# Performance work log

Measured on AMD Instinct MI355X. Metric: run time of the kernel, lower is better.

The kernel has to match this reference:

```python
import jax, jax.numpy as jnp
import numpy as np

B, N, C, CS, CP, H, L = 1, 2048, 128, 128, 16, 4, 3
NQ, NK = 32, 128  # local attention window: n_queries, n_keys
EPS = 1e-5


def _make_beta(n):
    l = np.arange(n)[:, None]
    m = np.arange(n)[None, :]
    con = np.zeros((n, n), dtype=bool)
    for c in np.arange(NQ / 2, n, NQ):
        con |= (np.abs(l - c) < NQ / 2) & (np.abs(m - c) < NK / 2)
    return np.where(con, 0.0, -1e10).astype(np.float32)


def setup_inputs() -> dict:
    key = jax.random.key(0)
    ks = iter(jax.random.split(key, 32))
    w = lambda *shape: jax.random.normal(next(ks), shape, dtype=jnp.float32) * 0.02
    inp = {
        'a': jax.random.normal(next(ks), (B, N, C), dtype=jnp.float32),
        's': jax.random.normal(next(ks), (B, N, CS), dtype=jnp.float32),
        'z': jax.random.normal(next(ks), (B, N, N, CP), dtype=jnp.float32),
        'beta': jnp.asarray(_make_beta(N))[None],
        'ada1_ln_w': jnp.ones((L, CS)), 'ada1_lin_w': w(L, CS, C),
        'ada1_lin_b': jnp.zeros((L, C)), 'ada1_nb_w': w(L, CS, C),
        'lnz_w': jnp.ones((L, CP)), 'lnz_b': jnp.zeros((L, CP)),
        'zinj_w': w(L, CP, H),
        'q_w': w(L, C, C), 'q_b': jnp.zeros((L, C)),
        'k_w': w(L, C, C), 'v_w': w(L, C, C),
        'g_w': w(L, C, C), 'o_w': w(L, C, C),
        'agate_w': w(L, CS, C), 'agate_b': jnp.full((L, C), -2.0),
        'ada2_ln_w': jnp.ones((L, CS)), 'ada2_lin_w': w(L, CS, C),
        'ada2_lin_b': jnp.zeros((L, C)), 'ada2_nb_w': w(L, CS, C),
        'lin1_w': w(L, C, 2 * C), 'lin2_w': w(L, C, 2 * C), 'lin3_w': w(L, 2 * C, C),
        'tgate_w': w(L, CS, C), 'tgate_b': jnp.full((L, C), -2.0),
    }
    return inp


def _ln(x):
    mu = jnp.mean(x, axis=-1, keepdims=True)
    var = jnp.var(x, axis=-1, keepdims=True)
    return (x - mu) * jax.lax.rsqrt(var + EPS)


def _adaln(a, s, ln_w, lin_w, lin_b, nb_w):
    # AdaLN: LN(a) gated & shifted by LN(s)
    a = _ln(a)
    sn = _ln(s) * ln_w
    return jax.nn.sigmoid(sn @ lin_w + lin_b) * a + sn @ nb_w


def _forward(a, s, z, beta, ada1_ln_w, ada1_lin_w, ada1_lin_b, ada1_nb_w,
             lnz_w, lnz_b, zinj_w, q_w, q_b, k_w, v_w, g_w, o_w,
             agate_w, agate_b, ada2_ln_w, ada2_lin_w, ada2_lin_b, ada2_nb_w,
             lin1_w, lin2_w, lin3_w, tgate_w, tgate_b):
    b_, n_, c_ = a.shape
    h_ = zinj_w.shape[-1]
    d_ = c_ // h_
    scale = 1.0 / np.sqrt(d_).astype(np.float32)
    zn0 = _ln(z)  # shared pre-affine LN of pair rep
    for i in range(q_w.shape[0]):
        # --- AttentionPairBias ---
        ah = _adaln(a, s, ada1_ln_w[i], ada1_lin_w[i], ada1_lin_b[i], ada1_nb_w[i])
        zb = jnp.einsum('bijc,ch->bhij', zn0 * lnz_w[i] + lnz_b[i], zinj_w[i])
        q = ((ah @ q_w[i] + q_b[i]) * scale).reshape(b_, n_, h_, d_)
        k = (ah @ k_w[i]).reshape(b_, n_, h_, d_)
        v = (ah @ v_w[i]).reshape(b_, n_, h_, d_)
        scores = jnp.einsum('bihd,bjhd->bhij', q, k) + zb + beta[:, None]
        p = jax.nn.softmax(scores, axis=-1)
        o = jnp.einsum('bhij,bjhd->bihd', p, v).reshape(b_, n_, c_)
        o = o * jax.nn.sigmoid(ah @ g_w[i])
        attn = (o @ o_w[i]) * jax.nn.sigmoid(s @ agate_w[i] + agate_b[i])
        # --- ConditionedTransitionBlock ---
        th = _adaln(a, s, ada2_ln_w[i], ada2_lin_w[i], ada2_lin_b[i], ada2_nb_w[i])
        bb = jax.nn.silu(th @ lin1_w[i]) * (th @ lin2_w[i])
        trans = jax.nn.sigmoid(s @ tgate_w[i] + tgate_b[i]) * th * (bb @ lin3_w[i])
        a = attn + trans
    return a


def reference(a, s, z, beta, ada1_ln_w, ada1_lin_w, ada1_lin_b, ada1_nb_w,
              lnz_w, lnz_b, zinj_w, q_w, q_b, k_w, v_w, g_w, o_w,
              agate_w, agate_b, ada2_ln_w, ada2_lin_w, ada2_lin_b, ada2_nb_w,
              lin1_w, lin2_w, lin3_w, tgate_w, tgate_b):
    return _forward(a, s, z, beta, ada1_ln_w, ada1_lin_w, ada1_lin_b, ada1_nb_w,
                    lnz_w, lnz_b, zinj_w, q_w, q_b, k_w, v_w, g_w, o_w,
                    agate_w, agate_b, ada2_ln_w, ada2_lin_w, ada2_lin_b, ada2_nb_w,
                    lin1_w, lin2_w, lin3_w, tgate_w, tgate_b)
```

## Files before the change

### kernel.cpp

```cpp
#include <hip/hip_runtime.h>


#define NT 2048

__device__ __forceinline__ float sig_(float x) { return 1.0f / (1.0f + __expf(-x)); }

__device__ __forceinline__ float redsum32(float v) {
#pragma unroll
  for (int o = 16; o > 0; o >>= 1) v += __shfl_xor(v, o);
  return v;
}

__device__ __forceinline__ void mm4(const float* __restrict__ W, int ldw,
                                    const float* As_row, int K, int c0, float* acc) {
  const float* __restrict__ wp = W + c0;
  for (int k = 0; k < K; k += 4) {
    float4 a4 = *(const float4*)(As_row + k);
#pragma unroll
    for (int kk = 0; kk < 4; ++kk) {
      float a = ((const float*)&a4)[kk];
      float4 w0 = *(const float4*)(wp);
      acc[0] = fmaf(a, w0.x, acc[0]);
      acc[1] = fmaf(a, w0.y, acc[1]);
      acc[2] = fmaf(a, w0.z, acc[2]);
      acc[3] = fmaf(a, w0.w, acc[3]);
      wp += ldw;
    }
  }
}

__device__ __forceinline__ void mm4x2(const float* __restrict__ W1,
                                      const float* __restrict__ W2, int ldw,
                                      const float* As_row, int K, int c0,
                                      float* acc1, float* acc2) {
  const float* __restrict__ wp1 = W1 + c0;
  const float* __restrict__ wp2 = W2 + c0;
  for (int k = 0; k < K; k += 4) {
    float4 a4 = *(const float4*)(As_row + k);
#pragma unroll
    for (int kk = 0; kk < 4; ++kk) {
      float a = ((const float*)&a4)[kk];
      float4 w0 = *(const float4*)(wp1);
      float4 u0 = *(const float4*)(wp2);
      acc1[0] = fmaf(a, w0.x, acc1[0]);
      acc1[1] = fmaf(a, w0.y, acc1[1]);
      acc1[2] = fmaf(a, w0.z, acc1[2]);
      acc1[3] = fmaf(a, w0.w, acc1[3]);
      acc2[0] = fmaf(a, u0.x, acc2[0]);
      acc2[1] = fmaf(a, u0.y, acc2[1]);
      acc2[2] = fmaf(a, u0.z, acc2[2]);
      acc2[3] = fmaf(a, u0.w, acc2[3]);
      wp1 += ldw; wp2 += ldw;
    }
  }
}

__device__ __forceinline__ void mm2(const float* __restrict__ W, int ldw,
                                    const float* As_row, int K, int c0, float* acc) {
  const float* __restrict__ wp = W + c0;
  for (int k = 0; k < K; k += 4) {
    float4 a4 = *(const float4*)(As_row + k);
#pragma unroll
    for (int kk = 0; kk < 4; ++kk) {
      float a = ((const float*)&a4)[kk];
      float2 w0 = *(const float2*)(wp);
      acc[0] = fmaf(a, w0.x, acc[0]);
      acc[1] = fmaf(a, w0.y, acc[1]);
      wp += ldw;
    }
  }
}

__global__ __launch_bounds__(256) void k_gates(
    const float* __restrict__ s, const float* __restrict__ agw,
    const float* __restrict__ agb, const float* __restrict__ tgw,
    const float* __restrict__ tgb, float* __restrict__ gatesA,
    float* __restrict__ gatesT) {
  __shared__ float As[8 * 132];
  int r0 = blockIdx.x * 8;
  int bz = blockIdx.y;
  int l = bz % 3, which = bz / 3;
  const float* W = (which ? tgw : agw) + (size_t)l * 128 * 128;
  const float* bias = (which ? tgb : agb) + (size_t)l * 128;
  float* outp = (which ? gatesT : gatesA) + (size_t)l * NT * 128;
  int tid = threadIdx.x;
  int r = tid >> 5, sub = tid & 31;
  *(float4*)&As[r * 132 + sub * 4] =
      *(const float4*)(s + (size_t)(r0 + r) * 128 + sub * 4);
  __syncthreads();
  int c0 = sub << 2;
  float acc[4] = {0, 0, 0, 0};
  mm4(W, 128, &As[r * 132], 128, c0, acc);
  size_t base = (size_t)(r0 + r) * 128 + c0;
#pragma unroll
  for (int j = 0; j < 4; ++j) outp[base + j] = sig_(acc[j] + bias[c0 + j]);
}

__global__ __launch_bounds__(256) void k_adaln12(
    const float* __restrict__ a, const float* __restrict__ s_in,
    const float* __restrict__ lnw1, const float* __restrict__ linw1,
    const float* __restrict__ linb1, const float* __restrict__ nbw1,
    const float* __restrict__ lnw2, const float* __restrict__ linw2,
    const float* __restrict__ linb2, const float* __restrict__ nbw2,
    float* __restrict__ ah, float* __restrict__ th) {
  __shared__ float Sn[8 * 132];
  __shared__ float La[8 * 132];
  int r0 = blockIdx.x * 8;
  int y = blockIdx.y;
  const float* lnw  = y ? lnw2 : lnw1;
  const float* linw = y ? linw2 : linw1;
  const float* linb = y ? linb2 : linb1;
  const float* nbw  = y ? nbw2 : nbw1;
  float* outp = y ? th : ah;
  int tid = threadIdx.x;
  int r = tid >> 5, sub = tid & 31;
  {
    float4 x = *(const float4*)(s_in + (size_t)(r0 + r) * 128 + sub * 4);
    float sm = redsum32(x.x + x.y + x.z + x.w);
    float mu = sm * (1.0f / 128.0f);
    float4 d = make_float4(x.x - mu, x.y - mu, x.z - mu, x.w - mu);
    float v = redsum32(d.x * d.x + d.y * d.y + d.z * d.z + d.w * d.w);
    float rs = rsqrtf(v * (1.0f / 128.0f) + 1e-5f);
    float4 sc = *(const float4*)(lnw + sub * 4);
    d.x *= rs * sc.x; d.y *= rs * sc.y; d.z *= rs * sc.z; d.w *= rs * sc.w;
    *(float4*)&Sn[r * 132 + sub * 4] = d;
  }
  {
    float4 x = *(const float4*)(a + (size_t)(r0 + r) * 128 + sub * 4);
    float sm = redsum32(x.x + x.y + x.z + x.w);
    float mu = sm * (1.0f / 128.0f);
    float4 d = make_float4(x.x - mu, x.y - mu, x.z - mu, x.w - mu);
    float v = redsum32(d.x * d.x + d.y * d.y + d.z * d.z + d.w * d.w);
    float rs = rsqrtf(v * (1.0f / 128.0f) + 1e-5f);
    d.x *= rs; d.y *= rs; d.z *= rs; d.w *= rs;
    *(float4*)&La[r * 132 + sub * 4] = d;
  }
  __syncthreads();
  int c0 = sub << 2;
  float acc1[4] = {0, 0, 0, 0}, acc2[4] = {0, 0, 0, 0};
  mm4x2(linw, nbw, 128, &Sn[r * 132], 128, c0, acc1, acc2);
  size_t base = (size_t)(r0 + r) * 128 + c0;
#pragma unroll
  for (int j = 0; j < 4; ++j) {
    float g = sig_(acc1[j] + linb[c0 + j]);
    outp[base + j] = g * La[r * 132 + c0 + j] + acc2[j];
  }
}

__global__ __launch_bounds__(256) void k_proj6(
    const float* __restrict__ ah, const float* __restrict__ th,
    const float* __restrict__ qw, const float* __restrict__ kw,
    const float* __restrict__ vw, const float* __restrict__ gw,
    const float* __restrict__ qb, const float* __restrict__ w1,
    const float* __restrict__ w2, float* __restrict__ qkvg,
    float* __restrict__ bb) {
  __shared__ float As[8 * 132];
  int r0 = blockIdx.x * 8;
  int y = blockIdx.y;
  int tid = threadIdx.x;
  int r = tid >> 5, sub = tid & 31;
  const float* src = (y < 4) ? ah : th;
  *(float4*)&As[r * 132 + sub * 4] =
      *(const float4*)(src + (size_t)(r0 + r) * 128 + sub * 4);
  __syncthreads();
  if (y < 4) {
    const float* W = (y == 0) ? qw : (y == 1) ? kw : (y == 2) ? vw : gw;
    int c0 = sub << 2;
    float acc[4] = {0, 0, 0, 0};
    mm4(W, 128, &As[r * 132], 128, c0, acc);
    float* op = qkvg + (size_t)(r0 + r) * 512 + y * 128 + c0;
    if (y == 0) {
#pragma unroll
      for (int j = 0; j < 4; ++j)
        op[j] = (acc[j] + qb[c0 + j]) * 0.17677669529663687f;
    } else if (y == 3) {
#pragma unroll
      for (int j = 0; j < 4; ++j) op[j] = sig_(acc[j]);
    } else {
#pragma unroll
      for (int j = 0; j < 4; ++j) op[j] = acc[j];
    }
  } else {
    int cb0 = (y - 4) * 128;
    int c0 = cb0 + (sub << 2);
    float acc1[4] = {0, 0, 0, 0}, acc2[4] = {0, 0, 0, 0};
    mm4x2(w1, w2, 256, &As[r * 132], 128, c0, acc1, acc2);
    size_t base = (size_t)(r0 + r) * 256 + c0;
#pragma unroll
    for (int j = 0; j < 4; ++j) {
      float x1 = acc1[j];
      bb[base + j] = x1 * sig_(x1) * acc2[j];
    }
  }
}

__global__ __launch_bounds__(256) void k_wattn(
    const float* __restrict__ qkvg, const float* __restrict__ z,
    const float* __restrict__ lnzw, const float* __restrict__ lnzb,
    const float* __restrict__ zinj, float* __restrict__ og,
    float* __restrict__ colpart) {
  __shared__ float Qs[8][128];
  __shared__ float S[8][4][132];
  __shared__ float KV[32][128];
  __shared__ float wz[4][16];
  __shared__ float bzw[2][4];
  __shared__ float red[2][128];

  const int tid = threadIdx.x;
  const int bx = blockIdx.x;
  if (bx >= 256) {
    int b = bx - 256;
    int rr = tid >> 7, c = tid & 127;
    float acc = 0.0f;
    for (int t = 0; t < 16; ++t) {
      int row = b * 32 + rr + t * 2;
      acc += qkvg[(size_t)row * 512 + 256 + c];
    }
    red[rr][c] = acc;
    __syncthreads();
    if (rr == 0) colpart[b * 128 + c] = red[0][c] + red[1][c];
    return;
  }

  const int win = bx >> 2, sub4 = bx & 3;
  const int cen = 16 + 32 * win;
  const int i0 = cen - 15 + 8 * sub4;
  const int nrows = (sub4 == 3) ? 7 : 8;
  const int jlo = max(0, cen - 63), jhi = min(2047, cen + 63);
  const int nk = jhi - jlo + 1;

  if (tid < 64) {
    int h = tid & 3, c = tid >> 2;
    wz[h][c] = lnzw[c] * zinj[c * 4 + h];
  }
  if (tid < 8) {
    int h = tid & 3, which = tid >> 2;
    float acc = 0.0f;
    for (int c = 0; c < 16; ++c) acc += (which ? lnzb[c] : lnzw[c]) * zinj[c * 4 + h];
    bzw[which][h] = acc;
  }
  {
    int r = tid >> 5, sub = tid & 31;
    int i = i0 + min(r, nrows - 1);
    *(float4*)&Qs[r][sub * 4] = *(const float4*)(qkvg + (size_t)i * 512 + sub * 4);
  }
  __syncthreads();

  for (int idx = tid; idx < 8 * 128; idx += 256) {
    int r = idx >> 7, jj = idx & 127;
    if (jj < nk) {
      int i = i0 + min(r, nrows - 1);
      int j = jlo + jj;
      const float* zp = z + ((size_t)i * 2048 + j) * 16;
      float x[16];
      *(float4*)&x[0]  = *(const float4*)(zp + 0);
      *(float4*)&x[4]  = *(const float4*)(zp + 4);
      *(float4*)&x[8]  = *(const float4*)(zp + 8);
      *(float4*)&x[12] = *(const float4*)(zp + 12);
      float sm = 0.0f;
#pragma unroll
      for (int c = 0; c < 16; ++c) sm += x[c];
      float mu = sm * (1.0f / 16.0f);
      float var = 0.0f;
#pragma unroll
      for (int c = 0; c < 16; ++c) { float d = x[c] - mu; var = fmaf(d, d, var); }
      float rs = rsqrtf(var * (1.0f / 16.0f) + 1e-5f);
#pragma unroll
      for (int h = 0; h < 4; ++h) {
        float dot = 0.0f;
#pragma unroll
        for (int c = 0; c < 16; ++c) dot = fmaf(x[c], wz[h][c], dot);
        S[r][h][jj] = fmaf(rs, dot - mu * bzw[0][h], bzw[1][h]);
      }
    } else {
#pragma unroll
      for (int h = 0; h < 4; ++h) S[r][h][jj] = -1e30f;
    }
  }
  __syncthreads();

  {
    const int r = tid >> 5, h = (tid >> 3) & 3, part = tid & 7;
    float qreg[32];
#pragma unroll
    for (int d4 = 0; d4 < 32; d4 += 4)
      *(float4*)&qreg[d4] = *(const float4*)&Qs[r][h * 32 + d4];
    for (int kb = 0; kb < 128; kb += 32) {
      for (int idx = tid; idx < 32 * 32; idx += 256) {
        int kk = idx >> 5, c4 = (idx & 31) << 2;
        int j = jlo + kb + kk;
        int cs = (c4 + ((kk >> 3) << 2)) & 127;
        float4 val = make_float4(0.f, 0.f, 0.f, 0.f);
        if (j <= jhi) val = *(const float4*)(qkvg + (size_t)j * 512 + 128 + c4);
        *(float4*)&KV[kk][cs] = val;
      }
      __syncthreads();
#pragma unroll
      for (int u = 0; u < 4; ++u) {
        int jj = part + (u << 3);
        int rot = (jj >> 3) << 2;
        float dot = 0.0f;
#pragma unroll
        for (int d4 = 0; d4 < 32; d4 += 4) {
          int cs = (h * 32 + d4 + rot) & 127;
          float4 kv = *(const float4*)&KV[jj][cs];
          dot = fmaf(qreg[d4 + 0], kv.x, dot);
          dot = fmaf(qreg[d4 + 1], kv.y, dot);
          dot = fmaf(qreg[d4 + 2], kv.z, dot);
          dot = fmaf(qreg[d4 + 3], kv.w, dot);
        }
        S[r][h][kb + jj] += dot;
      }
      __syncthreads();
    }
  }

  {
    const int rh = tid >> 3, part = tid & 7;
    const int sr = rh >> 2, sh = rh & 3;
    float* Srow = &S[sr][sh][0];
    float m = -1e30f;
#pragma unroll
    for (int st = 0; st < 16; ++st) m = fmaxf(m, Srow[part + (st << 3)]);
#pragma unroll
    for (int o = 4; o > 0; o >>= 1) m = fmaxf(m, __shfl_xor(m, o));
    float ss = 0.0f;
#pragma unroll
    for (int st = 0; st < 16; ++st) {
      int jj = part + (st << 3);
      float e = __expf(Srow[jj] - m);
      Srow[jj] = e;
      ss += e;
    }
#pragma unroll
    for (int o = 4; o > 0; o >>= 1) ss += __shfl_xor(ss, o);
    float inv = 1.0f / ss;
#pragma unroll
    for (int st = 0; st < 16; ++st) Srow[part + (st << 3)] *= inv;
  }
  __syncthreads();

  {
    const int r = tid >> 5, cg = tid & 31;
    const int ca = cg << 2;
    const int h = cg >> 3;
    float acc[4] = {0, 0, 0, 0};
    for (int kb = 0; kb < 128; kb += 32) {
      for (int idx = tid; idx < 32 * 32; idx += 256) {
        int kk = idx >> 5, c4 = (idx & 31) << 2;
        int j = jlo + kb + kk;
        int cs = (c4 + ((kk >> 3) << 2)) & 127;
        float4 val = make_float4(0.f, 0.f, 0.f, 0.f);
        if (j <= jhi) val = *(const float4*)(qkvg + (size_t)j * 512 + 256 + c4);
        *(float4*)&KV[kk][cs] = val;
      }
      __syncthreads();
#pragma unroll 4
      for (int kk = 0; kk < 32; ++kk) {
        int rot = (kk >> 3) << 2;
        float sa = S[r][h][kb + kk];
        float4 va = *(const float4*)&KV[kk][(ca + rot) & 127];
        acc[0] = fmaf(sa, va.x, acc[0]);
        acc[1] = fmaf(sa, va.y, acc[1]);
        acc[2] = fmaf(sa, va.z, acc[2]);
        acc[3] = fmaf(sa, va.w, acc[3]);
      }
      __syncthreads();
    }
    if (r < nrows) {
      int i = i0 + r;
      float4 ga = *(const float4*)(qkvg + (size_t)i * 512 + 384 + ca);
      float4 oa = make_float4(acc[0] * ga.x, acc[1] * ga.y, acc[2] * ga.z, acc[3] * ga.w);
      *(float4*)(og + (size_t)i * 128 + ca) = oa;
    }
  }
}

__global__ __launch_bounds__(512) void k_tail(
    const float* __restrict__ og, const float* __restrict__ ow,
    const float* __restrict__ gA, const float* __restrict__ colpart,
    const float* __restrict__ qkvg, const float* __restrict__ bbuf,
    const float* __restrict__ w3, const float* __restrict__ gT,
    const float* __restrict__ th, float* __restrict__ outp) {
  __shared__ float Ao[8 * 132];
  __shared__ float Bb[8 * 260];
  __shared__ float red[2][128];
  int r0 = blockIdx.x * 8;
  int tid = threadIdx.x;
  int r = tid >> 6, sub = tid & 63;
  if (sub < 32) {
    *(float4*)&Ao[r * 132 + sub * 4] =
        *(const float4*)(og + (size_t)(r0 + r) * 128 + sub * 4);
  }
  {
    *(float4*)&Bb[r * 260 + sub * 4] =
        *(const float4*)(bbuf + (size_t)(r0 + r) * 256 + sub * 4);
  }
  __syncthreads();
  if ((r0 & 31) == 0) {
    if (tid < 256) {
      int col = tid & 127, half = tid >> 7;
      float acc = 0.0f;
      for (int b = half; b < 64; b += 2) acc += colpart[b * 128 + col];
      red[half][col] = acc;
    }
    __syncthreads();
    if (tid < 128) {
      float mv = (red[0][tid] + red[1][tid]) * (1.0f / 2048.0f);
      Ao[tid] = mv * qkvg[(size_t)r0 * 512 + 384 + tid];
    }
    __syncthreads();
  }
  int c0 = sub << 1;
  float acc1[2] = {0, 0};
  mm2(ow, 128, &Ao[r * 132], 128, c0, acc1);
  float acc3[2] = {0, 0};
  mm2(w3, 128, &Bb[r * 260], 256, c0, acc3);
  size_t base = (size_t)(r0 + r) * 128 + c0;
#pragma unroll
  for (int j = 0; j < 2; ++j) {
    float attnv = acc1[j] * gA[base + j];
    outp[base + j] = attnv + gT[base + j] * th[base + j] * acc3[j];
  }
}

extern "C" void kernel_launch(void* const* d_in, const int* in_sizes, int n_in,
                              void* d_out, int out_size, void* d_ws, size_t ws_size,
                              hipStream_t stream) {
  (void)in_sizes; (void)n_in; (void)out_size; (void)ws_size;
  const float* A_in   = (const float*)d_in[0];
  const float* S_in   = (const float*)d_in[1];
  const float* Z_in   = (const float*)d_in[2];
  const float* ada1_ln_w  = (const float*)d_in[4];
  const float* ada1_lin_w = (const float*)d_in[5];
  const float* ada1_lin_b = (const float*)d_in[6];
  const float* ada1_nb_w  = (const float*)d_in[7];
  const float* lnz_w      = (const float*)d_in[8];
  const float* lnz_b      = (const float*)d_in[9];
  const float* zinj_w     = (const float*)d_in[10];
  const float* q_w        = (const float*)d_in[11];
  const float* q_b        = (const float*)d_in[12];
  const float* k_w        = (const float*)d_in[13];
  const float* v_w        = (const float*)d_in[14];
  const float* g_w        = (const float*)d_in[15];
  const float* o_w        = (const float*)d_in[16];
  const float* agate_w    = (const float*)d_in[17];
  const float* agate_b    = (const float*)d_in[18];
  const float* ada2_ln_w  = (const float*)d_in[19];
  const float* ada2_lin_w = (const float*)d_in[20];
  const float* ada2_lin_b = (const float*)d_in[21];
  const float* ada2_nb_w  = (const float*)d_in[22];
  const float* lin1_w     = (const float*)d_in[23];
  const float* lin2_w     = (const float*)d_in[24];
  const float* lin3_w     = (const float*)d_in[25];
  const float* tgate_w    = (const float*)d_in[26];
  const float* tgate_b    = (const float*)d_in[27];

  const int N = NT, C = 128;
  float* ws = (float*)d_ws;
  float* ah      = ws;
  float* th      = ah + (size_t)N * C;
  float* qkvg    = th + (size_t)N * C;
  float* og      = qkvg + (size_t)N * 512;
  float* bb      = og + (size_t)N * C;
  float* gatesA  = bb + (size_t)N * 256;
  float* gatesT  = gatesA + (size_t)3 * N * C;
  float* colpart = gatesT + (size_t)3 * N * C;

  dim3 blk(256);
  k_gates<<<dim3(256, 6), blk, 0, stream>>>(S_in, agate_w, agate_b, tgate_w,
                                            tgate_b, gatesA, gatesT);
  const float* acur = A_in;
  for (int l = 0; l < 3; ++l) {
    k_adaln12<<<dim3(256, 2), blk, 0, stream>>>(
        acur, S_in, ada1_ln_w + (size_t)l * C, ada1_lin_w + (size_t)l * C * C,
        ada1_lin_b + (size_t)l * C, ada1_nb_w + (size_t)l * C * C,
        ada2_ln_w + (size_t)l * C, ada2_lin_w + (size_t)l * C * C,
        ada2_lin_b + (size_t)l * C, ada2_nb_w + (size_t)l * C * C, ah, th);
    k_proj6<<<dim3(256, 6), blk, 0, stream>>>(
        ah, th, q_w + (size_t)l * C * C, k_w + (size_t)l * C * C,
        v_w + (size_t)l * C * C, g_w + (size_t)l * C * C, q_b + (size_t)l * C,
        lin1_w + (size_t)l * C * 2 * C, lin2_w + (size_t)l * C * 2 * C, qkvg, bb);
    k_wattn<<<320, blk, 0, stream>>>(qkvg, Z_in, lnz_w + (size_t)l * 16,
                                     lnz_b + (size_t)l * 16,
                                     zinj_w + (size_t)l * 64, og, colpart);
    k_tail<<<256, dim3(512), 0, stream>>>(og, o_w + (size_t)l * C * C,
                                          gatesA + (size_t)l * N * C, colpart,
                                          qkvg, bb, lin3_w + (size_t)l * 2 * C * C,
                                          gatesT + (size_t)l * N * C, th,
                                          (float*)d_out);
    acur = (const float*)d_out;
  }
}
```

Before: 730.5 us.

## Fuse AdaLN into projection kernel and halve attention rows per block

Merges the AdaLN kernel into the QKVG/transition projection kernel. Each of the six y-blocks recomputes its needed AdaLN output (ah or th) in shared memory instead of round-tripping it through global memory, which removes one launch per layer. This adds redundant AdaLN matmuls, since four blocks recompute ah and two recompute th. Separately, the windowed attention kernel now uses 4 query rows per block over 512 blocks, with 64-key tiles, to raise parallelism at the cost of more redundant z/K/V loads per row.

```diff
diff --git a/kernel.cpp b/kernel.cpp
--- a/kernel.cpp
+++ b/kernel.cpp
@@ -96,24 +96,29 @@
   for (int j = 0; j < 4; ++j) outp[base + j] = sig_(acc[j] + bias[c0 + j]);
 }
 
-__global__ __launch_bounds__(256) void k_adaln12(
+__global__ __launch_bounds__(256) void k_projf(
     const float* __restrict__ a, const float* __restrict__ s_in,
-    const float* __restrict__ lnw1, const float* __restrict__ linw1,
-    const float* __restrict__ linb1, const float* __restrict__ nbw1,
-    const float* __restrict__ lnw2, const float* __restrict__ linw2,
-    const float* __restrict__ linb2, const float* __restrict__ nbw2,
-    float* __restrict__ ah, float* __restrict__ th) {
+    const float* __restrict__ a1lnw, const float* __restrict__ a1linw,
+    const float* __restrict__ a1linb, const float* __restrict__ a1nbw,
+    const float* __restrict__ a2lnw, const float* __restrict__ a2linw,
+    const float* __restrict__ a2linb, const float* __restrict__ a2nbw,
+    const float* __restrict__ qw, const float* __restrict__ kw,
+    const float* __restrict__ vw, const float* __restrict__ gw,
+    const float* __restrict__ qb, const float* __restrict__ w1,
+    const float* __restrict__ w2, float* __restrict__ qkvg,
+    float* __restrict__ bb, float* __restrict__ th_out) {
   __shared__ float Sn[8 * 132];
   __shared__ float La[8 * 132];
+  __shared__ float Ah[8 * 132];
   int r0 = blockIdx.x * 8;
   int y = blockIdx.y;
-  const float* lnw  = y ? lnw2 : lnw1;
-  const float* linw = y ? linw2 : linw1;
-  const float* linb = y ? linb2 : linb1;
-  const float* nbw  = y ? nbw2 : nbw1;
-  float* outp = y ? th : ah;
   int tid = threadIdx.x;
   int r = tid >> 5, sub = tid & 31;
+  const bool is2 = (y >= 4);
+  const float* lnw  = is2 ? a2lnw : a1lnw;
+  const float* linw = is2 ? a2linw : a1linw;
+  const float* linb = is2 ? a2linb : a1linb;
+  const float* nbw  = is2 ? a2nbw : a1nbw;
   {
     float4 x = *(const float4*)(s_in + (size_t)(r0 + r) * 128 + sub * 4);
     float sm = redsum32(x.x + x.y + x.z + x.w);
@@ -137,37 +142,27 @@
   }
   __syncthreads();
   int c0 = sub << 2;
-  float acc1[4] = {0, 0, 0, 0}, acc2[4] = {0, 0, 0, 0};
-  mm4x2(linw, nbw, 128, &Sn[r * 132], 128, c0, acc1, acc2);
-  size_t base = (size_t)(r0 + r) * 128 + c0;
-#pragma unroll
-  for (int j = 0; j < 4; ++j) {
-    float g = sig_(acc1[j] + linb[c0 + j]);
-    outp[base + j] = g * La[r * 132 + c0 + j] + acc2[j];
-  }
-}
-
-__global__ __launch_bounds__(256) void k_proj6(
-    const float* __restrict__ ah, const float* __restrict__ th,
-    const float* __restrict__ qw, const float* __restrict__ kw,
-    const float* __restrict__ vw, const float* __restrict__ gw,
-    const float* __restrict__ qb, const float* __restrict__ w1,
-    const float* __restrict__ w2, float* __restrict__ qkvg,
-    float* __restrict__ bb) {
-  __shared__ float As[8 * 132];
-  int r0 = blockIdx.x * 8;
-  int y = blockIdx.y;
-  int tid = threadIdx.x;
-  int r = tid >> 5, sub = tid & 31;
-  const float* src = (y < 4) ? ah : th;
-  *(float4*)&As[r * 132 + sub * 4] =
-      *(const float4*)(src + (size_t)(r0 + r) * 128 + sub * 4);
+  {
+    float acc1[4] = {0, 0, 0, 0}, acc2[4] = {0, 0, 0, 0};
+    mm4x2(linw, nbw, 128, &Sn[r * 132], 128, c0, acc1, acc2);
+    float hv[4];
+#pragma unroll
+    for (int j = 0; j < 4; ++j) {
+      float g = sig_(acc1[j] + linb[c0 + j]);
+      hv[j] = g * La[r * 132 + c0 + j] + acc2[j];
+    }
+    *(float4*)&Ah[r * 132 + c0] = make_float4(hv[0], hv[1], hv[2], hv[3]);
+    if (y == 4) {
+      size_t base = (size_t)(r0 + r) * 128 + c0;
+#pragma unroll
+      for (int j = 0; j < 4; ++j) th_out[base + j] = hv[j];
+    }
+  }
   __syncthreads();
   if (y < 4) {
     const float* W = (y == 0) ? qw : (y == 1) ? kw : (y == 2) ? vw : gw;
-    int c0 = sub << 2;
     float acc[4] = {0, 0, 0, 0};
-    mm4(W, 128, &As[r * 132], 128, c0, acc);
+    mm4(W, 128, &Ah[r * 132], 128, c0, acc);
     float* op = qkvg + (size_t)(r0 + r) * 512 + y * 128 + c0;
     if (y == 0) {
 #pragma unroll
@@ -182,10 +177,10 @@
     }
   } else {
     int cb0 = (y - 4) * 128;
-    int c0 = cb0 + (sub << 2);
+    int cc0 = cb0 + c0;
     float acc1[4] = {0, 0, 0, 0}, acc2[4] = {0, 0, 0, 0};
-    mm4x2(w1, w2, 256, &As[r * 132], 128, c0, acc1, acc2);
-    size_t base = (size_t)(r0 + r) * 256 + c0;
+    mm4x2(w1, w2, 256, &Ah[r * 132], 128, cc0, acc1, acc2);
+    size_t base = (size_t)(r0 + r) * 256 + cc0;
 #pragma unroll
     for (int j = 0; j < 4; ++j) {
       float x1 = acc1[j];
@@ -199,17 +194,17 @@
     const float* __restrict__ lnzw, const float* __restrict__ lnzb,
     const float* __restrict__ zinj, float* __restrict__ og,
     float* __restrict__ colpart) {
-  __shared__ float Qs[8][128];
-  __shared__ float S[8][4][132];
-  __shared__ float KV[32][128];
+  __shared__ float Qs[4][128];
+  __shared__ float S[4][4][132];
+  __shared__ float KV[64][128];
   __shared__ float wz[4][16];
   __shared__ float bzw[2][4];
   __shared__ float red[2][128];
 
   const int tid = threadIdx.x;
   const int bx = blockIdx.x;
-  if (bx >= 256) {
-    int b = bx - 256;
+  if (bx >= 512) {
+    int b = bx - 512;
     int rr = tid >> 7, c = tid & 127;
     float acc = 0.0f;
     for (int t = 0; t < 16; ++t) {
@@ -222,10 +217,10 @@
     return;
   }
 
-  const int win = bx >> 2, sub4 = bx & 3;
+  const int win = bx >> 3, sub8 = bx & 7;
   const int cen = 16 + 32 * win;
-  const int i0 = cen - 15 + 8 * sub4;
-  const int nrows = (sub4 == 3) ? 7 : 8;
+  const int i0 = cen - 15 + 4 * sub8;
+  const int nrows = (sub8 == 7) ? 3 : 4;
   const int jlo = max(0, cen - 63), jhi = min(2047, cen + 63);
   const int nk = jhi - jlo + 1;
 
@@ -239,14 +234,14 @@
     for (int c = 0; c < 16; ++c) acc += (which ? lnzb[c] : lnzw[c]) * zinj[c * 4 + h];
     bzw[which][h] = acc;
   }
-  {
+  if (tid < 128) {
     int r = tid >> 5, sub = tid & 31;
     int i = i0 + min(r, nrows - 1);
     *(float4*)&Qs[r][sub * 4] = *(const float4*)(qkvg + (size_t)i * 512 + sub * 4);
   }
   __syncthreads();
 
-  for (int idx = tid; idx < 8 * 128; idx += 256) {
+  for (int idx = tid; idx < 4 * 128; idx += 256) {
     int r = idx >> 7, jj = idx & 127;
     if (jj < nk) {
       int i = i0 + min(r, nrows - 1);
@@ -280,13 +275,13 @@
   __syncthreads();
 
   {
-    const int r = tid >> 5, h = (tid >> 3) & 3, part = tid & 7;
+    const int r = tid >> 6, h = (tid >> 4) & 3, part = tid & 15;
     float qreg[32];
 #pragma unroll
     for (int d4 = 0; d4 < 32; d4 += 4)
       *(float4*)&qreg[d4] = *(const float4*)&Qs[r][h * 32 + d4];
-    for (int kb = 0; kb < 128; kb += 32) {
-      for (int idx = tid; idx < 32 * 32; idx += 256) {
+    for (int kb = 0; kb < 128; kb += 64) {
+      for (int idx = tid; idx < 64 * 32; idx += 256) {
         int kk = idx >> 5, c4 = (idx & 31) << 2;
         int j = jlo + kb + kk;
         int cs = (c4 + ((kk >> 3) << 2)) & 127;
@@ -297,7 +292,7 @@
       __syncthreads();
 #pragma unroll
       for (int u = 0; u < 4; ++u) {
-        int jj = part + (u << 3);
+        int jj = part + (u << 4);
         int rot = (jj >> 3) << 2;
         float dot = 0.0f;
 #pragma unroll
@@ -316,37 +311,37 @@
   }
 
   {
-    const int rh = tid >> 3, part = tid & 7;
+    const int rh = tid >> 4, part = tid & 15;
     const int sr = rh >> 2, sh = rh & 3;
     float* Srow = &S[sr][sh][0];
     float m = -1e30f;
 #pragma unroll
-    for (int st = 0; st < 16; ++st) m = fmaxf(m, Srow[part + (st << 3)]);
-#pragma unroll
-    for (int o = 4; o > 0; o >>= 1) m = fmaxf(m, __shfl_xor(m, o));
+    for (int st = 0; st < 8; ++st) m = fmaxf(m, Srow[part + (st << 4)]);
+#pragma unroll
+    for (int o = 8; o > 0; o >>= 1) m = fmaxf(m, __shfl_xor(m, o));
     float ss = 0.0f;
 #pragma unroll
-    for (int st = 0; st < 16; ++st) {
-      int jj = part + (st << 3);
+    for (int st = 0; st < 8; ++st) {
+      int jj = part + (st << 4);
       float e = __expf(Srow[jj] - m);
       Srow[jj] = e;
       ss += e;
     }
 #pragma unroll
-    for (int o = 4; o > 0; o >>= 1) ss += __shfl_xor(ss, o);
+    for (int o = 8; o > 0; o >>= 1) ss += __shfl_xor(ss, o);
     float inv = 1.0f / ss;
 #pragma unroll
-    for (int st = 0; st < 16; ++st) Srow[part + (st << 3)] *= inv;
-  }
-  __syncthreads();
-
-  {
-    const int r = tid >> 5, cg = tid & 31;
-    const int ca = cg << 2;
-    const int h = cg >> 3;
-    float acc[4] = {0, 0, 0, 0};
-    for (int kb = 0; kb < 128; kb += 32) {
-      for (int idx = tid; idx < 32 * 32; idx += 256) {
+    for (int st = 0; st < 8; ++st) Srow[part + (st << 4)] *= inv;
+  }
+  __syncthreads();
+
+  {
+    const int r = tid >> 6, cg = tid & 63;
+    const int ca = cg << 1;
+    const int h = cg >> 4;
+    float acc[2] = {0, 0};
+    for (int kb = 0; kb < 128; kb += 64) {
+      for (int idx = tid; idx < 64 * 32; idx += 256) {
         int kk = idx >> 5, c4 = (idx & 31) << 2;
         int j = jlo + kb + kk;
         int cs = (c4 + ((kk >> 3) << 2)) & 127;
@@ -355,23 +350,21 @@
         *(float4*)&KV[kk][cs] = val;
       }
       __syncthreads();
-#pragma unroll 4
-      for (int kk = 0; kk < 32; ++kk) {
+#pragma unroll 8
+      for (int kk = 0; kk < 64; ++kk) {
         int rot = (kk >> 3) << 2;
         float sa = S[r][h][kb + kk];
-        float4 va = *(const float4*)&KV[kk][(ca + rot) & 127];
+        float2 va = *(const float2*)&KV[kk][(ca + rot) & 127];
         acc[0] = fmaf(sa, va.x, acc[0]);
         acc[1] = fmaf(sa, va.y, acc[1]);
-        acc[2] = fmaf(sa, va.z, acc[2]);
-        acc[3] = fmaf(sa, va.w, acc[3]);
       }
       __syncthreads();
     }
     if (r < nrows) {
       int i = i0 + r;
-      float4 ga = *(const float4*)(qkvg + (size_t)i * 512 + 384 + ca);
-      float4 oa = make_float4(acc[0] * ga.x, acc[1] * ga.y, acc[2] * ga.z, acc[3] * ga.w);
-      *(float4*)(og + (size_t)i * 128 + ca) = oa;
+      float2 ga = *(const float2*)(qkvg + (size_t)i * 512 + 384 + ca);
+      float2 oa = make_float2(acc[0] * ga.x, acc[1] * ga.y);
+      *(float2*)(og + (size_t)i * 128 + ca) = oa;
     }
   }
 }
@@ -458,8 +451,7 @@
 
   const int N = NT, C = 128;
   float* ws = (float*)d_ws;
-  float* ah      = ws;
-  float* th      = ah + (size_t)N * C;
+  float* th      = ws;
   float* qkvg    = th + (size_t)N * C;
   float* og      = qkvg + (size_t)N * 512;
   float* bb      = og + (size_t)N * C;
@@ -472,16 +464,16 @@
                                             tgate_b, gatesA, gatesT);
   const float* acur = A_in;
   for (int l = 0; l < 3; ++l) {
-    k_adaln12<<<dim3(256, 2), blk, 0, stream>>>(
+    k_projf<<<dim3(256, 6), blk, 0, stream>>>(
         acur, S_in, ada1_ln_w + (size_t)l * C, ada1_lin_w + (size_t)l * C * C,
         ada1_lin_b + (size_t)l * C, ada1_nb_w + (size_t)l * C * C,
         ada2_ln_w + (size_t)l * C, ada2_lin_w + (size_t)l * C * C,
-        ada2_lin_b + (size_t)l * C, ada2_nb_w + (size_t)l * C * C, ah, th);
-    k_proj6<<<dim3(256, 6), blk, 0, stream>>>(
-        ah, th, q_w + (size_t)l * C * C, k_w + (size_t)l * C * C,
+        ada2_lin_b + (size_t)l * C, ada2_nb_w + (size_t)l * C * C,
+        q_w + (size_t)l * C * C, k_w + (size_t)l * C * C,
         v_w + (size_t)l * C * C, g_w + (size_t)l * C * C, q_b + (size_t)l * C,
-        lin1_w + (size_t)l * C * 2 * C, lin2_w + (size_t)l * C * 2 * C, qkvg, bb);
-    k_wattn<<<320, blk, 0, stream>>>(qkvg, Z_in, lnz_w + (size_t)l * 16,
+        lin1_w + (size_t)l * C * 2 * C, lin2_w + (size_t)l * C * 2 * C,
+        qkvg, bb, th);
+    k_wattn<<<576, blk, 0, stream>>>(qkvg, Z_in, lnz_w + (size_t)l * 16,
                                      lnz_b + (size_t)l * 16,
                                      zinj_w + (size_t)l * 64, og, colpart);
     k_tail<<<256, dim3(512), 0, stream>>>(og, o_w + (size_t)l * C * C,
```

Result: slower. 786.9 us (+7.7%).

## Fuse AdaLN into gate kernel and into previous layer's tail kernel

Applied to the files above, without the earlier changes.

The per-layer AdaLN kernel is removed. Layer 0's AdaLN for both the attention and transition inputs now runs as extra grid rows of the gate-precompute kernel. For layers 1 and 2, the tail kernel of the previous layer computes it right after writing the layer output, using 64-lane reductions for the layer norms and a new 2-column matmul helper that folds in the LN scale. This removes launches and a global round-trip of the layer output. In exchange, the tail kernel carries more register and shared-memory pressure, and it reads and writes th in place under __restrict__.

```diff
diff --git a/kernel.cpp b/kernel.cpp
--- a/kernel.cpp
+++ b/kernel.cpp
@@ -8,6 +8,12 @@
 __device__ __forceinline__ float redsum32(float v) {
 #pragma unroll
   for (int o = 16; o > 0; o >>= 1) v += __shfl_xor(v, o);
+  return v;
+}
+
+__device__ __forceinline__ float redsum64(float v) {
+#pragma unroll
+  for (int o = 32; o > 0; o >>= 1) v += __shfl_xor(v, o);
   return v;
 }
 
@@ -71,79 +77,98 @@
   }
 }
 
-__global__ __launch_bounds__(256) void k_gates(
+__device__ __forceinline__ void mm2x2s(const float* __restrict__ W1,
+                                       const float* __restrict__ W2, int ldw,
+                                       const float* As_row,
+                                       const float* __restrict__ lnw, int c0,
+                                       float* acc1, float* acc2) {
+  const float* __restrict__ wp1 = W1 + c0;
+  const float* __restrict__ wp2 = W2 + c0;
+  for (int k = 0; k < 128; k += 4) {
+    float4 a4 = *(const float4*)(As_row + k);
+    float4 s4 = *(const float4*)(lnw + k);
+    a4.x *= s4.x; a4.y *= s4.y; a4.z *= s4.z; a4.w *= s4.w;
+#pragma unroll
+    for (int kk = 0; kk < 4; ++kk) {
+      float a = ((const float*)&a4)[kk];
+      float2 w0 = *(const float2*)(wp1);
+      float2 u0 = *(const float2*)(wp2);
+      acc1[0] = fmaf(a, w0.x, acc1[0]);
+      acc1[1] = fmaf(a, w0.y, acc1[1]);
+      acc2[0] = fmaf(a, u0.x, acc2[0]);
+      acc2[1] = fmaf(a, u0.y, acc2[1]);
+      wp1 += ldw; wp2 += ldw;
+    }
+  }
+}
+
+__global__ __launch_bounds__(256) void k_gatesA(
     const float* __restrict__ s, const float* __restrict__ agw,
     const float* __restrict__ agb, const float* __restrict__ tgw,
     const float* __restrict__ tgb, float* __restrict__ gatesA,
-    float* __restrict__ gatesT) {
+    float* __restrict__ gatesT, const float* __restrict__ a,
+    const float* __restrict__ a1lnw, const float* __restrict__ a1linw,
+    const float* __restrict__ a1linb, const float* __restrict__ a1nbw,
+    const float* __restrict__ a2lnw, const float* __restrict__ a2linw,
+    const float* __restrict__ a2linb, const float* __restrict__ a2nbw,
+    float* __restrict__ ah, float* __restrict__ th) {
   __shared__ float As[8 * 132];
+  __shared__ float La[8 * 132];
   int r0 = blockIdx.x * 8;
   int bz = blockIdx.y;
-  int l = bz % 3, which = bz / 3;
-  const float* W = (which ? tgw : agw) + (size_t)l * 128 * 128;
-  const float* bias = (which ? tgb : agb) + (size_t)l * 128;
-  float* outp = (which ? gatesT : gatesA) + (size_t)l * NT * 128;
   int tid = threadIdx.x;
   int r = tid >> 5, sub = tid & 31;
-  *(float4*)&As[r * 132 + sub * 4] =
-      *(const float4*)(s + (size_t)(r0 + r) * 128 + sub * 4);
-  __syncthreads();
   int c0 = sub << 2;
-  float acc[4] = {0, 0, 0, 0};
-  mm4(W, 128, &As[r * 132], 128, c0, acc);
-  size_t base = (size_t)(r0 + r) * 128 + c0;
-#pragma unroll
-  for (int j = 0; j < 4; ++j) outp[base + j] = sig_(acc[j] + bias[c0 + j]);
-}
-
-__global__ __launch_bounds__(256) void k_adaln12(
-    const float* __restrict__ a, const float* __restrict__ s_in,
-    const float* __restrict__ lnw1, const float* __restrict__ linw1,
-    const float* __restrict__ linb1, const float* __restrict__ nbw1,
-    const float* __restrict__ lnw2, const float* __restrict__ linw2,
-    const float* __restrict__ linb2, const float* __restrict__ nbw2,
-    float* __restrict__ ah, float* __restrict__ th) {
-  __shared__ float Sn[8 * 132];
-  __shared__ float La[8 * 132];
-  int r0 = blockIdx.x * 8;
-  int y = blockIdx.y;
-  const float* lnw  = y ? lnw2 : lnw1;
-  const float* linw = y ? linw2 : linw1;
-  const float* linb = y ? linb2 : linb1;
-  const float* nbw  = y ? nbw2 : nbw1;
-  float* outp = y ? th : ah;
-  int tid = threadIdx.x;
-  int r = tid >> 5, sub = tid & 31;
-  {
-    float4 x = *(const float4*)(s_in + (size_t)(r0 + r) * 128 + sub * 4);
-    float sm = redsum32(x.x + x.y + x.z + x.w);
-    float mu = sm * (1.0f / 128.0f);
-    float4 d = make_float4(x.x - mu, x.y - mu, x.z - mu, x.w - mu);
-    float v = redsum32(d.x * d.x + d.y * d.y + d.z * d.z + d.w * d.w);
-    float rs = rsqrtf(v * (1.0f / 128.0f) + 1e-5f);
-    float4 sc = *(const float4*)(lnw + sub * 4);
-    d.x *= rs * sc.x; d.y *= rs * sc.y; d.z *= rs * sc.z; d.w *= rs * sc.w;
-    *(float4*)&Sn[r * 132 + sub * 4] = d;
-  }
-  {
-    float4 x = *(const float4*)(a + (size_t)(r0 + r) * 128 + sub * 4);
-    float sm = redsum32(x.x + x.y + x.z + x.w);
-    float mu = sm * (1.0f / 128.0f);
-    float4 d = make_float4(x.x - mu, x.y - mu, x.z - mu, x.w - mu);
-    float v = redsum32(d.x * d.x + d.y * d.y + d.z * d.z + d.w * d.w);
-    float rs = rsqrtf(v * (1.0f / 128.0f) + 1e-5f);
-    d.x *= rs; d.y *= rs; d.z *= rs; d.w *= rs;
-    *(float4*)&La[r * 132 + sub * 4] = d;
-  }
-  __syncthreads();
-  int c0 = sub << 2;
-  float acc1[4] = {0, 0, 0, 0}, acc2[4] = {0, 0, 0, 0};
-  mm4x2(linw, nbw, 128, &Sn[r * 132], 128, c0, acc1, acc2);
-  size_t base = (size_t)(r0 + r) * 128 + c0;
-#pragma unroll
-  for (int j = 0; j < 4; ++j) {
-    float g = sig_(acc1[j] + linb[c0 + j]);
-    outp[base + j] = g * La[r * 132 + c0 + j] + acc2[j];
+  if (bz < 6) {
+    int l = bz % 3, which = bz / 3;
+    const float* W = (which ? tgw : agw) + (size_t)l * 128 * 128;
+    const float* bias = (which ? tgb : agb) + (size_t)l * 128;
+    float* outp = (which ? gatesT : gatesA) + (size_t)l * NT * 128;
+    *(float4*)&As[r * 132 + sub * 4] =
+        *(const float4*)(s + (size_t)(r0 + r) * 128 + sub * 4);
+    __syncthreads();
+    float acc[4] = {0, 0, 0, 0};
+    mm4(W, 128, &As[r * 132], 128, c0, acc);
+    size_t base = (size_t)(r0 + r) * 128 + c0;
+#pragma unroll
+    for (int j = 0; j < 4; ++j) outp[base + j] = sig_(acc[j] + bias[c0 + j]);
+  } else {
+    int y2 = bz - 6;
+    const float* lnw  = y2 ? a2lnw : a1lnw;
+    const float* linw = y2 ? a2linw : a1linw;
+    const float* linb = y2 ? a2linb : a1linb;
+    const float* nbw  = y2 ? a2nbw : a1nbw;
+    float* outp = y2 ? th : ah;
+    {
+      float4 x = *(const float4*)(s + (size_t)(r0 + r) * 128 + sub * 4);
+      float sm = redsum32(x.x + x.y + x.z + x.w);
+      float mu = sm * (1.0f / 128.0f);
+      float4 d = make_float4(x.x - mu, x.y - mu, x.z - mu, x.w - mu);
+      float v = redsum32(d.x * d.x + d.y * d.y + d.z * d.z + d.w * d.w);
+      float rs = rsqrtf(v * (1.0f / 128.0f) + 1e-5f);
+      float4 sc = *(const float4*)(lnw + sub * 4);
+      d.x *= rs * sc.x; d.y *= rs * sc.y; d.z *= rs * sc.z; d.w *= rs * sc.w;
+      *(float4*)&As[r * 132 + sub * 4] = d;
+    }
+    {
+      float4 x = *(const float4*)(a + (size_t)(r0 + r) * 128 + sub * 4);
+      float sm = redsum32(x.x + x.y + x.z + x.w);
+      float mu = sm * (1.0f / 128.0f);
+      float4 d = make_float4(x.x - mu, x.y - mu, x.z - mu, x.w - mu);
+      float v = redsum32(d.x * d.x + d.y * d.y + d.z * d.z + d.w * d.w);
+      float rs = rsqrtf(v * (1.0f / 128.0f) + 1e-5f);
+      d.x *= rs; d.y *= rs; d.z *= rs; d.w *= rs;
+      *(float4*)&La[r * 132 + sub * 4] = d;
+    }
+    __syncthreads();
+    float acc1[4] = {0, 0, 0, 0}, acc2[4] = {0, 0, 0, 0};
+    mm4x2(linw, nbw, 128, &As[r * 132], 128, c0, acc1, acc2);
+    size_t base = (size_t)(r0 + r) * 128 + c0;
+#pragma unroll
+    for (int j = 0; j < 4; ++j) {
+      float g = sig_(acc1[j] + linb[c0 + j]);
+      outp[base + j] = g * La[r * 132 + c0 + j] + acc2[j];
+    }
   }
 }
 
@@ -376,14 +401,21 @@
   }
 }
 
-__global__ __launch_bounds__(512) void k_tail(
+__global__ __launch_bounds__(512) void k_tailA(
     const float* __restrict__ og, const float* __restrict__ ow,
     const float* __restrict__ gA, const float* __restrict__ colpart,
     const float* __restrict__ qkvg, const float* __restrict__ bbuf,
     const float* __restrict__ w3, const float* __restrict__ gT,
-    const float* __restrict__ th, float* __restrict__ outp) {
+    const float* __restrict__ th, float* __restrict__ outp,
+    const float* __restrict__ s_in,
+    const float* __restrict__ a1lnw, const float* __restrict__ a1linw,
+    const float* __restrict__ a1linb, const float* __restrict__ a1nbw,
+    const float* __restrict__ a2lnw, const float* __restrict__ a2linw,
+    const float* __restrict__ a2linb, const float* __restrict__ a2nbw,
+    float* __restrict__ ah_out, float* __restrict__ th_out, int do_next) {
   __shared__ float Ao[8 * 132];
   __shared__ float Bb[8 * 260];
+  __shared__ float SnR[8 * 132];
   __shared__ float red[2][128];
   int r0 = blockIdx.x * 8;
   int tid = threadIdx.x;
@@ -417,10 +449,47 @@
   float acc3[2] = {0, 0};
   mm2(w3, 128, &Bb[r * 260], 256, c0, acc3);
   size_t base = (size_t)(r0 + r) * 128 + c0;
-#pragma unroll
-  for (int j = 0; j < 2; ++j) {
-    float attnv = acc1[j] * gA[base + j];
-    outp[base + j] = attnv + gT[base + j] * th[base + j] * acc3[j];
+  float ov0, ov1;
+  {
+    float a0 = acc1[0] * gA[base + 0];
+    float a1 = acc1[1] * gA[base + 1];
+    ov0 = a0 + gT[base + 0] * th[base + 0] * acc3[0];
+    ov1 = a1 + gT[base + 1] * th[base + 1] * acc3[1];
+    outp[base + 0] = ov0;
+    outp[base + 1] = ov1;
+  }
+  if (!do_next) return;
+  float la0, la1;
+  {
+    float sm = redsum64(ov0 + ov1);
+    float mu = sm * (1.0f / 128.0f);
+    float d0 = ov0 - mu, d1 = ov1 - mu;
+    float vv = redsum64(d0 * d0 + d1 * d1);
+    float rs = rsqrtf(vv * (1.0f / 128.0f) + 1e-5f);
+    la0 = d0 * rs; la1 = d1 * rs;
+  }
+  {
+    float s0 = s_in[base + 0], s1 = s_in[base + 1];
+    float sm = redsum64(s0 + s1);
+    float mu = sm * (1.0f / 128.0f);
+    float e0 = s0 - mu, e1 = s1 - mu;
+    float vv = redsum64(e0 * e0 + e1 * e1);
+    float rs = rsqrtf(vv * (1.0f / 128.0f) + 1e-5f);
+    SnR[r * 132 + c0] = e0 * rs;
+    SnR[r * 132 + c0 + 1] = e1 * rs;
+  }
+  __syncthreads();
+  {
+    float p1[2] = {0, 0}, p2[2] = {0, 0};
+    mm2x2s(a1linw, a1nbw, 128, &SnR[r * 132], a1lnw, c0, p1, p2);
+    ah_out[base + 0] = sig_(p1[0] + a1linb[c0 + 0]) * la0 + p2[0];
+    ah_out[base + 1] = sig_(p1[1] + a1linb[c0 + 1]) * la1 + p2[1];
+  }
+  {
+    float p1[2] = {0, 0}, p2[2] = {0, 0};
+    mm2x2s(a2linw, a2nbw, 128, &SnR[r * 132], a2lnw, c0, p1, p2);
+    th_out[base + 0] = sig_(p1[0] + a2linb[c0 + 0]) * la0 + p2[0];
+    th_out[base + 1] = sig_(p1[1] + a2linb[c0 + 1]) * la1 + p2[1];
   }
 }
 
@@ -468,27 +537,28 @@
   float* colpart = gatesT + (size_t)3 * N * C;
 
   dim3 blk(256);
-  k_gates<<<dim3(256, 6), blk, 0, stream>>>(S_in, agate_w, agate_b, tgate_w,
-                                            tgate_b, gatesA, gatesT);
-  const float* acur = A_in;
+  k_gatesA<<<dim3(256, 8), blk, 0, stream>>>(
+      S_in, agate_w, agate_b, tgate_w, tgate_b, gatesA, gatesT, A_in,
+      ada1_ln_w, ada1_lin_w, ada1_lin_b, ada1_nb_w,
+      ada2_ln_w, ada2_lin_w, ada2_lin_b, ada2_nb_w, ah, th);
   for (int l = 0; l < 3; ++l) {
-    k_adaln12<<<dim3(256, 2), blk, 0, stream>>>(
-        acur, S_in, ada1_ln_w + (size_t)l * C, ada1_lin_w + (size_t)l * C * C,
-        ada1_lin_b + (size_t)l * C, ada1_nb_w + (size_t)l * C * C,
-        ada2_ln_w + (size_t)l * C, ada2_lin_w + (size_t)l * C * C,
-        ada2_lin_b + (size_t)l * C, ada2_nb_w + (size_t)l * C * C, ah, th);
     k_proj6<<<dim3(256, 6), blk, 0, stream>>>(
         ah, th, q_w + (size_t)l * C * C, k_w + (size_t)l * C * C,
         v_w + (size_t)l * C * C, g_w + (size_t)l * C * C, q_b + (size_t)l * C,
-        lin1_w + (size_t)l * C * 2 * C, lin2_w + (size_t)l * C * 2 * C, qkvg, bb);
+        lin1_w + (size_t)l * C * 2 * C, lin2_w + (size_t)l * C * 2 * C,
+        qkvg, bb);
     k_wattn<<<320, blk, 0, stream>>>(qkvg, Z_in, lnz_w + (size_t)l * 16,
                                      lnz_b + (size_t)l * 16,
                                      zinj_w + (size_t)l * 64, og, colpart);
-    k_tail<<<256, dim3(512), 0, stream>>>(og, o_w + (size_t)l * C * C,
-                                          gatesA + (size_t)l * N * C, colpart,
-                                          qkvg, bb, lin3_w + (size_t)l * 2 * C * C,
-                                          gatesT + (size_t)l * N * C, th,
-                                          (float*)d_out);
-    acur = (const float*)d_out;
-  }
-}
+    int nl = (l < 2) ? (l + 1) : 2;
+    k_tailA<<<256, dim3(512), 0, stream>>>(
+        og, o_w + (size_t)l * C * C, gatesA + (size_t)l * N * C, colpart, qkvg,
+        bb, lin3_w + (size_t)l * 2 * C * C, gatesT + (size_t)l * N * C, th,
+        (float*)d_out, S_in,
+        ada1_ln_w + (size_t)nl * C, ada1_lin_w + (size_t)nl * C * C,
+        ada1_lin_b + (size_t)nl * C, ada1_nb_w + (size_t)nl * C * C,
+        ada2_ln_w + (size_t)nl * C, ada2_lin_w + (size_t)nl * C * C,
+        ada2_lin_b + (size_t)nl * C, ada2_nb_w + (size_t)nl * C * C,
+        ah, th, (l < 2) ? 1 : 0);
+  }
+}
```

Result: no change. 737.2 us (+0.9%).
